# Kernel tuning notes

Measured on AMD Instinct MI355X. Metric: run time of the kernel, lower is better.

Reference implementation:

```python
import jax, jax.numpy as jnp
import numpy as np

N = 200000   # nodes
E = 6400000  # edges
F = 128      # input node features
H = 6        # hiddenSize (module constant)
C = 10       # num_classes
G = 64       # graphs in batch


def setup_inputs() -> dict:
    key = jax.random.key(0)
    ks = jax.random.split(key, 7)
    x = jax.random.normal(ks[0], (N, F), dtype=jnp.float32)
    edge_index = jax.random.randint(ks[1], (2, E), 0, N, dtype=jnp.int32)
    batch = jnp.sort(jax.random.randint(ks[2], (N,), 0, G, dtype=jnp.int32))
    W1 = jax.random.normal(ks[3], (F, H), dtype=jnp.float32) * (1.0 / np.sqrt(F))
    b1 = jnp.zeros((H,), dtype=jnp.float32)
    W2 = jax.random.normal(ks[4], (H, C), dtype=jnp.float32) * (1.0 / np.sqrt(H))
    b2 = jnp.zeros((C,), dtype=jnp.float32)
    return {"x": x, "edge_index": edge_index, "batch": batch,
            "W1": W1, "b1": b1, "W2": W2, "b2": b2}


def _gcn_conv(x, W, b, row, col, dis):
    # PyG GCNConv: h = x W; out = D^{-1/2}(A+I)D^{-1/2} h + b
    h = x @ W                                      # [N, out]
    norm = dis[row] * dis[col]                     # [E] edge normalization
    msg = norm[:, None] * h[row]                   # gather from source nodes
    agg = jax.ops.segment_sum(msg, col, num_segments=N)  # scatter-add to targets
    # self-loop term: norm = dis[i]*dis[i]
    return agg + (dis * dis)[:, None] * h + b


def reference(x, edge_index, batch, W1, b1, W2, b2):
    row, col = edge_index[0], edge_index[1]
    # degree after adding self-loops (edge_weight = 1)
    deg = jax.ops.segment_sum(jnp.ones((E,), dtype=x.dtype), col, num_segments=N) + 1.0
    dis = jax.lax.rsqrt(deg)                       # deg^{-1/2}

    h = _gcn_conv(x, W1, b1, row, col, dis)
    h = jax.nn.relu(h)
    # dropout is identity in inference mode
    h = _gcn_conv(h, W2, b2, row, col, dis)        # [N, C]

    # global mean pool over each graph
    sums = jax.ops.segment_sum(h, batch, num_segments=G)                  # [G, C]
    cnts = jax.ops.segment_sum(jnp.ones((N,), dtype=h.dtype), batch, num_segments=G)
    pooled = sums / jnp.maximum(cnts, 1.0)[:, None]
    return jax.nn.log_softmax(pooled, axis=1)      # [G, C]
```

## Files before the change

### kernel.cpp

```cpp
#include <hip/hip_runtime.h>
#include <math.h>

#define N_NODES 200000
#define N_EDGES 6400000
#define F_IN    128
#define H_HID   6
#define C_OUT   10
#define G_BATCH 64

#define TILE_E  8192
#define NT      ((N_EDGES + TILE_E - 1) / TILE_E)
#define EPT     16
#define BSH     9
#define BNODES  512
#define NBUCK   ((N_NODES + BNODES - 1) / BNODES)
#define BCAP    17408
#define XBLK    512
#define NXB     ((N_NODES + XBLK - 1) / XBLK)

__device__ __forceinline__ unsigned short f2bf(float f) {
    unsigned u = __float_as_uint(f);
    u += 0x7fff + ((u >> 16) & 1);
    return (unsigned short)(u >> 16);
}
__device__ __forceinline__ unsigned pack2(float a, float b) {
    return (unsigned)f2bf(a) | ((unsigned)f2bf(b) << 16);
}
__device__ __forceinline__ float bf_lo(unsigned u) { return __uint_as_float(u << 16); }
__device__ __forceinline__ float bf_hi(unsigned u) { return __uint_as_float(u & 0xffff0000u); }

__global__ __launch_bounds__(512, 8) void megaA_kernel(const int* __restrict__ row,
                                                       const int* __restrict__ col,
                                                       const float* __restrict__ x,
                                                       const float* __restrict__ W1,
                                                       int* __restrict__ gcur,
                                                       int* __restrict__ binned,
                                                       float* __restrict__ xacc, int E) {
    __shared__ int sortbuf[TILE_E];
    __shared__ int cnt[512];
    __shared__ int pos[513];
    __shared__ int lbase[512];
    __shared__ int wtot[8];
    int tid = threadIdx.x;
    int bid = blockIdx.x;

    if ((bid % 3 == 0) && (bid / 3 < NXB)) {
        float* w = (float*)sortbuf;
        for (int i = tid; i < F_IN * H_HID; i += 512) w[i] = W1[i];
        __syncthreads();
        int n = (bid / 3) * XBLK + tid;
        if (n >= N_NODES) return;
        float acc[H_HID] = {0.f, 0.f, 0.f, 0.f, 0.f, 0.f};
        const float4* xr = (const float4*)(x + (size_t)n * F_IN);
#pragma unroll 4
        for (int f4 = 0; f4 < F_IN / 4; ++f4) {
            float4 v = xr[f4];
            int f = f4 * 4;
#pragma unroll
            for (int j = 0; j < H_HID; ++j) {
                acc[j] += v.x * w[(f + 0) * H_HID + j] + v.y * w[(f + 1) * H_HID + j]
                        + v.z * w[(f + 2) * H_HID + j] + v.w * w[(f + 3) * H_HID + j];
            }
        }
#pragma unroll
        for (int j = 0; j < H_HID; ++j) xacc[j * N_NODES + n] = acc[j];
        return;
    }

    int nxb_before = (bid + 2) / 3;
    int t = bid - (nxb_before < NXB ? nxb_before : NXB);
    int base = t * TILE_E;
    int tile_n = min(TILE_E, E - base);

    cnt[tid] = 0;
    __syncthreads();

    int myval[EPT];
    int myb[EPT];
    int ebase = base + tid * EPT;
    if (ebase + EPT <= E) {
        const int4* c4 = (const int4*)(col + ebase);
        const int4* r4 = (const int4*)(row + ebase);
#pragma unroll
        for (int q = 0; q < EPT / 4; ++q) {
            int4 c = c4[q];
            int4 r = r4[q];
            int k = q * 4;
            myval[k + 0] = ((c.x & (BNODES - 1)) << 18) | r.x;  myb[k + 0] = c.x >> BSH;
            myval[k + 1] = ((c.y & (BNODES - 1)) << 18) | r.y;  myb[k + 1] = c.y >> BSH;
            myval[k + 2] = ((c.z & (BNODES - 1)) << 18) | r.z;  myb[k + 2] = c.z >> BSH;
            myval[k + 3] = ((c.w & (BNODES - 1)) << 18) | r.w;  myb[k + 3] = c.w >> BSH;
        }
#pragma unroll
        for (int k = 0; k < EPT; ++k) atomicAdd(&cnt[myb[k]], 1);
    } else {
#pragma unroll
        for (int k = 0; k < EPT; ++k) {
            int e = ebase + k;
            if (e < E) {
                int c = col[e];
                myval[k] = ((c & (BNODES - 1)) << 18) | row[e];
                myb[k] = c >> BSH;
                atomicAdd(&cnt[myb[k]], 1);
            } else {
                myb[k] = -1;
            }
        }
    }
    __syncthreads();

    int c = cnt[tid];
    int v = c;
    int lane = tid & 63, wid = tid >> 6;
#pragma unroll
    for (int off = 1; off < 64; off <<= 1) {
        int u = __shfl_up(v, off);
        if (lane >= off) v += u;
    }
    if (lane == 63) wtot[wid] = v;
    __syncthreads();
    if (tid == 0) {
        int running = 0;
#pragma unroll
        for (int i = 0; i < 8; ++i) { int w2 = wtot[i]; wtot[i] = running; running += w2; }
    }
    __syncthreads();
    int incl = v + wtot[wid];
    int excl = incl - c;
    pos[tid] = excl;
    cnt[tid] = excl;
    if (tid == 511) pos[512] = incl;
    if (tid < NBUCK) {
        lbase[tid] = tid * BCAP + (c ? atomicAdd(&gcur[tid], c) : 0);
    }
    __syncthreads();

#pragma unroll
    for (int k = 0; k < EPT; ++k) {
        if (myb[k] >= 0) {
            int p = atomicAdd(&cnt[myb[k]], 1);
            sortbuf[p] = myval[k];
        }
    }
    __syncthreads();

    for (int i = tid; i < tile_n; i += 512) {
        int lo = 0, hi = NBUCK - 1;
        while (lo < hi) {
            int mid = (lo + hi + 1) >> 1;
            if (pos[mid] <= i) lo = mid; else hi = mid - 1;
        }
        binned[lbase[lo] + (i - pos[lo])] = sortbuf[i];
    }
}

__global__ __launch_bounds__(1024) void passB2_kernel(const int* __restrict__ gcur,
                                                      const int* __restrict__ binned,
                                                      const float* __restrict__ xacc,
                                                      int* __restrict__ deg,
                                                      uint4* __restrict__ h1b) {
    __shared__ int cnt[512];
    int b = blockIdx.x, tid = threadIdx.x;
    int bb = b * BCAP, be = bb + gcur[b];
    if (tid < 512) cnt[tid] = 0;
    __syncthreads();
    int e = bb + tid;
    for (; e + 3072 < be; e += 4096) {
        int p0 = binned[e], p1 = binned[e + 1024], p2 = binned[e + 2048], p3 = binned[e + 3072];
        atomicAdd(&cnt[p0 >> 18], 1); atomicAdd(&cnt[p1 >> 18], 1);
        atomicAdd(&cnt[p2 >> 18], 1); atomicAdd(&cnt[p3 >> 18], 1);
    }
    for (; e < be; e += 1024) atomicAdd(&cnt[binned[e] >> 18], 1);
    __syncthreads();
    if (tid < 512) {
        int n = (b << BSH) + tid;
        if (n < N_NODES) {
            int dv = cnt[tid];
            deg[n] = dv;
            float d = rsqrtf((float)dv + 1.0f);
            float a0 = xacc[0 * N_NODES + n], a1 = xacc[1 * N_NODES + n];
            float a2 = xacc[2 * N_NODES + n], a3 = xacc[3 * N_NODES + n];
            float a4 = xacc[4 * N_NODES + n], a5 = xacc[5 * N_NODES + n];
            uint4 o;
            o.x = pack2(d * a0, d * a1);
            o.y = pack2(d * a2, d * a3);
            o.z = pack2(d * a4, d * a5);
            o.w = __float_as_uint(d);
            h1b[n] = o;
        }
    }
}

#define DEG_SCAN(INCL)                                                          \
    {                                                                           \
        int n0 = (b << BSH) + tid;                                              \
        int v0 = (tid < 512 && n0 < N_NODES) ? deg[n0] : 0;                     \
        int v = v0;                                                             \
        int lane = tid & 63, wid = tid >> 6;                                    \
        _Pragma("unroll")                                                       \
        for (int off = 1; off < 64; off <<= 1) {                                \
            int u = __shfl_up(v, off);                                          \
            if (lane >= off) v += u;                                            \
        }                                                                       \
        if (wid < 8 && lane == 63) wtot[wid] = v;                               \
        __syncthreads();                                                        \
        if (tid == 0) {                                                         \
            int running = 0;                                                    \
            _Pragma("unroll")                                                   \
            for (int i = 0; i < 8; ++i) { int w2 = wtot[i]; wtot[i] = running; running += w2; } \
        }                                                                       \
        __syncthreads();                                                        \
        if (tid < 512) cnt[tid] = v + wtot[wid] - (INCL ? 0 : v0);              \
    }                                                                           \
    __syncthreads();

#define GATHER_BODY(TBL)                                                        \
    float a[H_HID] = {0.f, 0.f, 0.f, 0.f, 0.f, 0.f};                            \
    {                                                                           \
        int ee = s + sub;                                                       \
        for (; ee + 24 < e_end; ee += 32) {                                     \
            int i0 = stage[ee], i1 = stage[ee + 8];                             \
            int i2 = stage[ee + 16], i3 = stage[ee + 24];                       \
            uint4 v0 = TBL[i0], v1 = TBL[i1], v2 = TBL[i2], v3 = TBL[i3];       \
            a[0] += (bf_lo(v0.x) + bf_lo(v1.x)) + (bf_lo(v2.x) + bf_lo(v3.x));  \
            a[1] += (bf_hi(v0.x) + bf_hi(v1.x)) + (bf_hi(v2.x) + bf_hi(v3.x));  \
            a[2] += (bf_lo(v0.y) + bf_lo(v1.y)) + (bf_lo(v2.y) + bf_lo(v3.y));  \
            a[3] += (bf_hi(v0.y) + bf_hi(v1.y)) + (bf_hi(v2.y) + bf_hi(v3.y));  \
            a[4] += (bf_lo(v0.z) + bf_lo(v1.z)) + (bf_lo(v2.z) + bf_lo(v3.z));  \
            a[5] += (bf_hi(v0.z) + bf_hi(v1.z)) + (bf_hi(v2.z) + bf_hi(v3.z));  \
        }                                                                       \
        for (; ee < e_end; ee += 8) {                                           \
            uint4 vv = TBL[stage[ee]];                                          \
            a[0] += bf_lo(vv.x); a[1] += bf_hi(vv.x);                           \
            a[2] += bf_lo(vv.y); a[3] += bf_hi(vv.y);                           \
            a[4] += bf_lo(vv.z); a[5] += bf_hi(vv.z);                           \
        }                                                                       \
    }                                                                           \
    _Pragma("unroll")                                                           \
    for (int j = 0; j < H_HID; ++j) {                                           \
        _Pragma("unroll")                                                       \
        for (int off = 4; off > 0; off >>= 1) a[j] += __shfl_xor(a[j], off);    \
    }

__global__ __launch_bounds__(1024) void bg1_kernel(const int* __restrict__ gcur,
                                                   const int* __restrict__ binned,
                                                   const int* __restrict__ deg,
                                                   const uint4* __restrict__ h1b,
                                                   const float* __restrict__ b1,
                                                   int* __restrict__ csr,
                                                   uint4* __restrict__ rs) {
    __shared__ int stage[BCAP];
    __shared__ int cnt[512];
    __shared__ int wtot[8];
    int b = blockIdx.x, tid = threadIdx.x;
    int bb = b * BCAP, be = bb + gcur[b];
    int total = be - bb;

    DEG_SCAN(0)

    {
        int e = bb + tid;
        for (; e + 3072 < be; e += 4096) {
            int p0 = binned[e], p1 = binned[e + 1024];
            int p2 = binned[e + 2048], p3 = binned[e + 3072];
            int s0 = atomicAdd(&cnt[p0 >> 18], 1); stage[s0] = p0 & 0x3FFFF;
            int s1 = atomicAdd(&cnt[p1 >> 18], 1); stage[s1] = p1 & 0x3FFFF;
            int s2 = atomicAdd(&cnt[p2 >> 18], 1); stage[s2] = p2 & 0x3FFFF;
            int s3 = atomicAdd(&cnt[p3 >> 18], 1); stage[s3] = p3 & 0x3FFFF;
        }
        for (; e < be; e += 1024) {
            int p = binned[e];
            int s = atomicAdd(&cnt[p >> 18], 1); stage[s] = p & 0x3FFFF;
        }
    }
    __syncthreads();

    for (int i = tid * 4; i + 3 < total; i += 4096)
        *(int4*)(csr + bb + i) = *(const int4*)(stage + i);
    {
        int b4 = total & ~3, r = total - b4;
        if (tid < r) csr[bb + b4 + tid] = stage[b4 + tid];
    }

    int sub = tid & 7, grp = tid >> 3;
    for (int ch = 0; ch < 4; ++ch) {
        int ln = ch * 128 + grp;
        int n = (b << BSH) + ln;
        int s = ln ? cnt[ln - 1] : 0;
        int e_end = cnt[ln];
        GATHER_BODY(h1b)
        if (sub == 0 && n < N_NODES) {
            uint4 self = h1b[n];
            float d = __uint_as_float(self.w);
            float sf[H_HID] = {bf_lo(self.x), bf_hi(self.x), bf_lo(self.y),
                               bf_hi(self.y), bf_lo(self.z), bf_hi(self.z)};
            float r[H_HID];
#pragma unroll
            for (int j = 0; j < H_HID; ++j) {
                float vv = d * (a[j] + sf[j]) + b1[j];
                r[j] = d * (vv > 0.f ? vv : 0.f);
            }
            uint4 o;
            o.x = pack2(r[0], r[1]);
            o.y = pack2(r[2], r[3]);
            o.z = pack2(r[4], r[5]);
            o.w = self.w;
            rs[n] = o;
        }
    }
}

__global__ __launch_bounds__(1024) void bg2_kernel(const int* __restrict__ gcur,
                                                   const int* __restrict__ deg,
                                                   const int* __restrict__ csr,
                                                   const uint4* __restrict__ rs,
                                                   const float* __restrict__ W2,
                                                   const int* __restrict__ batch,
                                                   float* __restrict__ sums) {
    __shared__ int stage[BCAP];
    __shared__ int cnt[512];
    __shared__ int wtot[8];
    __shared__ float w2s[H_HID * C_OUT];
    __shared__ float nv[128][C_OUT + 1];
    __shared__ int lg[128];
    __shared__ float gacc[2][C_OUT];
    __shared__ int sg0;
    int b = blockIdx.x, tid = threadIdx.x;
    int bb = b * BCAP;
    int total = gcur[b];
    if (tid < H_HID * C_OUT) w2s[tid] = W2[tid];
    if (tid < 2 * C_OUT) ((float*)gacc)[tid] = 0.f;
    if (tid == 0) sg0 = batch[b << BSH];

    for (int i = tid * 4; i + 3 < total; i += 4096)
        *(int4*)(stage + i) = *(const int4*)(csr + bb + i);
    {
        int b4 = total & ~3, r = total - b4;
        if (tid < r) stage[b4 + tid] = csr[bb + b4 + tid];
    }

    DEG_SCAN(1)

    int sub = tid & 7, grp = tid >> 3;
    for (int ch = 0; ch < 4; ++ch) {
        int ln = ch * 128 + grp;
        int n = (b << BSH) + ln;
        int s = ln ? cnt[ln - 1] : 0;
        int e_end = cnt[ln];
        GATHER_BODY(rs)
        uint4 self = {0u, 0u, 0u, 0u};
        if (n < N_NODES) self = rs[n];
        float d = (n < N_NODES) ? __uint_as_float(self.w) : 0.f;
        float t[H_HID] = {a[0] + bf_lo(self.x), a[1] + bf_hi(self.x),
                          a[2] + bf_lo(self.y), a[3] + bf_hi(self.y),
                          a[4] + bf_lo(self.z), a[5] + bf_hi(self.z)};
        {
            float accv = 0.f;
#pragma unroll
            for (int j = 0; j < H_HID; ++j) accv += t[j] * w2s[j * C_OUT + sub];
            nv[grp][sub] = d * accv;
            if (sub < 2) {
                float accv2 = 0.f;
#pragma unroll
                for (int j = 0; j < H_HID; ++j) accv2 += t[j] * w2s[j * C_OUT + sub + 8];
                nv[grp][sub + 8] = d * accv2;
            }
        }
        if (sub == 0) lg[grp] = (n < N_NODES) ? batch[n] : sg0;
        __syncthreads();
        if (tid < 80) {
            int seg = tid / C_OUT, cc = tid - seg * C_OUT;
            int g = -1; float av = 0.f;
            for (int i = 0; i < 16; ++i) {
                int wdx = seg * 16 + i;
                int gw = lg[wdx];
                if (gw != g) {
                    if (g >= 0) {
                        int r2 = g - sg0;
                        if (r2 < 2) atomicAdd(&gacc[r2][cc], av);
                        else atomicAdd(&sums[g * C_OUT + cc], av);
                    }
                    g = gw; av = 0.f;
                }
                av += nv[wdx][cc];
            }
            int r2 = g - sg0;
            if (r2 < 2) atomicAdd(&gacc[r2][cc], av);
            else atomicAdd(&sums[g * C_OUT + cc], av);
        }
        __syncthreads();
    }
    if (tid < 2 * C_OUT) {
        int r2 = tid / C_OUT, cc = tid - r2 * C_OUT;
        int g = sg0 + r2;
        if (g < G_BATCH) atomicAdd(&sums[g * C_OUT + cc], gacc[r2][cc]);
    }
}

__global__ void pool_finish_kernel(const float* __restrict__ sums, const int* __restrict__ batch,
                                   const float* __restrict__ b2, float* __restrict__ out) {
    int g = threadIdx.x;
    if (g >= G_BATCH) return;
    int lo = 0, hi = N_NODES;
    while (lo < hi) { int mid = (lo + hi) >> 1; if (batch[mid] < g) lo = mid + 1; else hi = mid; }
    int c0 = lo;
    hi = N_NODES;
    while (lo < hi) { int mid = (lo + hi) >> 1; if (batch[mid] < g + 1) lo = mid + 1; else hi = mid; }
    float inv = 1.0f / fmaxf((float)(lo - c0), 1.0f);
    float v[C_OUT], m = -INFINITY;
#pragma unroll
    for (int c = 0; c < C_OUT; ++c) {
        v[c] = sums[g * C_OUT + c] * inv + b2[c];
        m = fmaxf(m, v[c]);
    }
    float s = 0.f;
#pragma unroll
    for (int c = 0; c < C_OUT; ++c) s += expf(v[c] - m);
    float lse = m + logf(s);
#pragma unroll
    for (int c = 0; c < C_OUT; ++c) out[g * C_OUT + c] = v[c] - lse;
}

extern "C" void kernel_launch(void* const* d_in, const int* in_sizes, int n_in,
                              void* d_out, int out_size, void* d_ws, size_t ws_size,
                              hipStream_t stream) {
    const float* x   = (const float*)d_in[0];
    const int* ei    = (const int*)d_in[1];
    const int* row   = ei;
    const int* col   = ei + N_EDGES;
    const int* batch = (const int*)d_in[2];
    const float* W1  = (const float*)d_in[3];
    const float* b1  = (const float*)d_in[4];
    const float* W2  = (const float*)d_in[5];
    const float* b2  = (const float*)d_in[6];
    float* out = (float*)d_out;

    char* p = (char*)d_ws;
    float* sums   = (float*)p;  p += (size_t)G_BATCH * C_OUT * 4;
    int*   gcur   = (int*)p;    p += (size_t)400 * 4;
    int*   deg    = (int*)p;    p += (size_t)N_NODES * 4;
    int*   binned = (int*)p;    p += (size_t)NBUCK * BCAP * 4;
    int*   csr    = (int*)p;    p += (size_t)NBUCK * BCAP * 4;
    float* xacc   = (float*)p;  p += (size_t)H_HID * N_NODES * 4;
    uint4* h1b    = (uint4*)p;  p += (size_t)N_NODES * 16;
    uint4* rs     = (uint4*)p;

    hipMemsetAsync(sums, 0, (size_t)G_BATCH * C_OUT * 4 + 400 * 4, stream);

    megaA_kernel  <<<NT + NXB, 512, 0, stream>>>(row, col, x, W1, gcur, binned, xacc, N_EDGES);
    passB2_kernel <<<NBUCK, 1024, 0, stream>>>(gcur, binned, xacc, deg, h1b);
    bg1_kernel    <<<NBUCK, 1024, 0, stream>>>(gcur, binned, deg, h1b, b1, csr, rs);
    bg2_kernel    <<<NBUCK, 1024, 0, stream>>>(gcur, deg, csr, rs, W2, batch, sums);
    pool_finish_kernel<<<1, 64, 0, stream>>>(sums, batch, b2, out);
}
```

Before: 327.0 us.

## Halve bucket size to 256 nodes and reorder node-transform blocks after sort tiles

Nodes are now bucketed in groups of 256 instead of 512. This doubles the number of buckets and blocks, and roughly halves the per-block shared staging buffer in the gather kernels, so more blocks can be resident per CU and load balance improves. The edge-binning kernel now tracks 1024 bucket counters, with each thread scanning two buckets. The x·W1 blocks are moved to after all sort tiles instead of being interleaved. The risks are more global atomics on bucket cursors, more scattered binned writes, and a tighter per-bucket capacity margin.

```diff
diff --git a/kernel.cpp b/kernel.cpp
--- a/kernel.cpp
+++ b/kernel.cpp
@@ -11,10 +11,10 @@
 #define TILE_E  8192
 #define NT      ((N_EDGES + TILE_E - 1) / TILE_E)
 #define EPT     16
-#define BSH     9
-#define BNODES  512
+#define BSH     8
+#define BNODES  256
 #define NBUCK   ((N_NODES + BNODES - 1) / BNODES)
-#define BCAP    17408
+#define BCAP    9216
 #define XBLK    512
 #define NXB     ((N_NODES + XBLK - 1) / XBLK)
 
@@ -37,18 +37,18 @@
                                                        int* __restrict__ binned,
                                                        float* __restrict__ xacc, int E) {
     __shared__ int sortbuf[TILE_E];
-    __shared__ int cnt[512];
-    __shared__ int pos[513];
-    __shared__ int lbase[512];
+    __shared__ int cnt[1024];
+    __shared__ int pos[1024];
+    __shared__ int lbase[1024];
     __shared__ int wtot[8];
     int tid = threadIdx.x;
     int bid = blockIdx.x;
 
-    if ((bid % 3 == 0) && (bid / 3 < NXB)) {
+    if (bid >= NT) {
         float* w = (float*)sortbuf;
         for (int i = tid; i < F_IN * H_HID; i += 512) w[i] = W1[i];
         __syncthreads();
-        int n = (bid / 3) * XBLK + tid;
+        int n = (bid - NT) * XBLK + tid;
         if (n >= N_NODES) return;
         float acc[H_HID] = {0.f, 0.f, 0.f, 0.f, 0.f, 0.f};
         const float4* xr = (const float4*)(x + (size_t)n * F_IN);
@@ -67,12 +67,12 @@
         return;
     }
 
-    int nxb_before = (bid + 2) / 3;
-    int t = bid - (nxb_before < NXB ? nxb_before : NXB);
+    int t = bid;
     int base = t * TILE_E;
     int tile_n = min(TILE_E, E - base);
 
     cnt[tid] = 0;
+    cnt[tid + 512] = 0;
     __syncthreads();
 
     int myval[EPT];
@@ -109,8 +109,9 @@
     }
     __syncthreads();
 
-    int c = cnt[tid];
-    int v = c;
+    int a0 = cnt[2 * tid], a1 = cnt[2 * tid + 1];
+    int s = a0 + a1;
+    int v = s;
     int lane = tid & 63, wid = tid >> 6;
 #pragma unroll
     for (int off = 1; off < 64; off <<= 1) {
@@ -125,13 +126,15 @@
         for (int i = 0; i < 8; ++i) { int w2 = wtot[i]; wtot[i] = running; running += w2; }
     }
     __syncthreads();
-    int incl = v + wtot[wid];
-    int excl = incl - c;
-    pos[tid] = excl;
-    cnt[tid] = excl;
-    if (tid == 511) pos[512] = incl;
-    if (tid < NBUCK) {
-        lbase[tid] = tid * BCAP + (c ? atomicAdd(&gcur[tid], c) : 0);
+    {
+        int pairExcl = v + wtot[wid] - s;
+        pos[2 * tid] = pairExcl;
+        pos[2 * tid + 1] = pairExcl + a0;
+        cnt[2 * tid] = pairExcl;
+        cnt[2 * tid + 1] = pairExcl + a0;
+        int b0 = 2 * tid, b1 = 2 * tid + 1;
+        if (b0 < NBUCK) lbase[b0] = b0 * BCAP + (a0 ? atomicAdd(&gcur[b0], a0) : 0);
+        if (b1 < NBUCK) lbase[b1] = b1 * BCAP + (a1 ? atomicAdd(&gcur[b1], a1) : 0);
     }
     __syncthreads();
 
@@ -159,10 +162,10 @@
                                                       const float* __restrict__ xacc,
                                                       int* __restrict__ deg,
                                                       uint4* __restrict__ h1b) {
-    __shared__ int cnt[512];
+    __shared__ int cnt[BNODES];
     int b = blockIdx.x, tid = threadIdx.x;
     int bb = b * BCAP, be = bb + gcur[b];
-    if (tid < 512) cnt[tid] = 0;
+    if (tid < BNODES) cnt[tid] = 0;
     __syncthreads();
     int e = bb + tid;
     for (; e + 3072 < be; e += 4096) {
@@ -172,7 +175,7 @@
     }
     for (; e < be; e += 1024) atomicAdd(&cnt[binned[e] >> 18], 1);
     __syncthreads();
-    if (tid < 512) {
+    if (tid < BNODES) {
         int n = (b << BSH) + tid;
         if (n < N_NODES) {
             int dv = cnt[tid];
@@ -194,7 +197,7 @@
 #define DEG_SCAN(INCL)                                                          \
     {                                                                           \
         int n0 = (b << BSH) + tid;                                              \
-        int v0 = (tid < 512 && n0 < N_NODES) ? deg[n0] : 0;                     \
+        int v0 = (tid < BNODES && n0 < N_NODES) ? deg[n0] : 0;                  \
         int v = v0;                                                             \
         int lane = tid & 63, wid = tid >> 6;                                    \
         _Pragma("unroll")                                                       \
@@ -202,15 +205,15 @@
             int u = __shfl_up(v, off);                                          \
             if (lane >= off) v += u;                                            \
         }                                                                       \
-        if (wid < 8 && lane == 63) wtot[wid] = v;                               \
+        if (wid < 4 && lane == 63) wtot[wid] = v;                               \
         __syncthreads();                                                        \
         if (tid == 0) {                                                         \
             int running = 0;                                                    \
             _Pragma("unroll")                                                   \
-            for (int i = 0; i < 8; ++i) { int w2 = wtot[i]; wtot[i] = running; running += w2; } \
+            for (int i = 0; i < 4; ++i) { int w2 = wtot[i]; wtot[i] = running; running += w2; } \
         }                                                                       \
         __syncthreads();                                                        \
-        if (tid < 512) cnt[tid] = v + wtot[wid] - (INCL ? 0 : v0);              \
+        if (tid < BNODES) cnt[tid] = v + wtot[wid] - (INCL ? 0 : v0);           \
     }                                                                           \
     __syncthreads();
 
@@ -250,8 +253,8 @@
                                                    int* __restrict__ csr,
                                                    uint4* __restrict__ rs) {
     __shared__ int stage[BCAP];
-    __shared__ int cnt[512];
-    __shared__ int wtot[8];
+    __shared__ int cnt[BNODES];
+    __shared__ int wtot[4];
     int b = blockIdx.x, tid = threadIdx.x;
     int bb = b * BCAP, be = bb + gcur[b];
     int total = be - bb;
@@ -283,7 +286,7 @@
     }
 
     int sub = tid & 7, grp = tid >> 3;
-    for (int ch = 0; ch < 4; ++ch) {
+    for (int ch = 0; ch < 2; ++ch) {
         int ln = ch * 128 + grp;
         int n = (b << BSH) + ln;
         int s = ln ? cnt[ln - 1] : 0;
@@ -318,8 +321,8 @@
                                                    const int* __restrict__ batch,
                                                    float* __restrict__ sums) {
     __shared__ int stage[BCAP];
-    __shared__ int cnt[512];
-    __shared__ int wtot[8];
+    __shared__ int cnt[BNODES];
+    __shared__ int wtot[4];
     __shared__ float w2s[H_HID * C_OUT];
     __shared__ float nv[128][C_OUT + 1];
     __shared__ int lg[128];
@@ -342,7 +345,7 @@
     DEG_SCAN(1)
 
     int sub = tid & 7, grp = tid >> 3;
-    for (int ch = 0; ch < 4; ++ch) {
+    for (int ch = 0; ch < 2; ++ch) {
         int ln = ch * 128 + grp;
         int n = (b << BSH) + ln;
         int s = ln ? cnt[ln - 1] : 0;
@@ -437,7 +440,7 @@
 
     char* p = (char*)d_ws;
     float* sums   = (float*)p;  p += (size_t)G_BATCH * C_OUT * 4;
-    int*   gcur   = (int*)p;    p += (size_t)400 * 4;
+    int*   gcur   = (int*)p;    p += (size_t)800 * 4;
     int*   deg    = (int*)p;    p += (size_t)N_NODES * 4;
     int*   binned = (int*)p;    p += (size_t)NBUCK * BCAP * 4;
     int*   csr    = (int*)p;    p += (size_t)NBUCK * BCAP * 4;
@@ -445,7 +448,7 @@
     uint4* h1b    = (uint4*)p;  p += (size_t)N_NODES * 16;
     uint4* rs     = (uint4*)p;
 
-    hipMemsetAsync(sums, 0, (size_t)G_BATCH * C_OUT * 4 + 400 * 4, stream);
+    hipMemsetAsync(sums, 0, (size_t)G_BATCH * C_OUT * 4 + 800 * 4, stream);
 
     megaA_kernel  <<<NT + NXB, 512, 0, stream>>>(row, col, x, W1, gcur, binned, xacc, N_EDGES);
     passB2_kernel <<<NBUCK, 1024, 0, stream>>>(gcur, binned, xacc, deg, h1b);
```

New measurement: 339.8 us. 3.9% more time.
